# Kernel tuning notes

Hardware: AMD Instinct MI355X
Metric: run time of the kernel (lower is better)

Reference implementation:

```python
import jax, jax.numpy as jnp
import numpy as np

V, H, E, L = 50257, 1024, 1024, 512


def setup_inputs() -> dict:
    key = jax.random.key(0)
    ks = jax.random.split(key, 16)
    s = 0.02  # init scale
    return {
        "input_token": jax.random.randint(ks[0], (1,), 0, V),
        "hidden": jax.random.normal(ks[1], (1, 1, H), jnp.float32),
        "encoder_outputs": jax.random.normal(ks[2], (L, H), jnp.float32),
        "embedding": jax.random.normal(ks[3], (V, E), jnp.float32) * s,
        "attn_w": jax.random.normal(ks[4], (L, H + E), jnp.float32) * s,
        "attn_b": jnp.zeros((L,), jnp.float32),
        "comb_w": jax.random.normal(ks[5], (E, H + E), jnp.float32) * s,
        "comb_b": jnp.zeros((E,), jnp.float32),
        "w_ih": jax.random.normal(ks[6], (3 * H, E), jnp.float32) * s,
        "w_hh": jax.random.normal(ks[7], (3 * H, H), jnp.float32) * s,
        "b_ih": jnp.zeros((3 * H,), jnp.float32),
        "b_hh": jnp.zeros((3 * H,), jnp.float32),
        "out_w": jax.random.normal(ks[8], (V, H), jnp.float32) * s,
        "out_b": jnp.zeros((V,), jnp.float32),
    }


def reference(input_token, hidden, encoder_outputs, embedding, attn_w, attn_b,
              comb_w, comb_b, w_ih, w_hh, b_ih, b_hh, out_w, out_b):
    # embedded = embedding(input).view(1,1,-1); dropout is identity in eval
    emb = embedding[input_token].reshape(1, E)            # [1, E]
    h0 = hidden[0]                                        # [1, H]
    # attention over encoder positions
    attn_logits = jnp.concatenate([emb, h0], axis=1) @ attn_w.T + attn_b  # [1, L]
    attn_weights = jax.nn.softmax(attn_logits, axis=1)
    attn_applied = attn_weights @ encoder_outputs         # [1, H]
    # combine + relu
    x = jnp.concatenate([emb, attn_applied], axis=1) @ comb_w.T + comb_b  # [1, E]
    x = jax.nn.relu(x)
    # single GRU cell step (PyTorch gate order: r, z, n)
    gi = x @ w_ih.T + b_ih                                # [1, 3H]
    gh = h0 @ w_hh.T + b_hh                               # [1, 3H]
    i_r, i_z, i_n = jnp.split(gi, 3, axis=1)
    h_r, h_z, h_n = jnp.split(gh, 3, axis=1)
    r = jax.nn.sigmoid(i_r + h_r)
    z = jax.nn.sigmoid(i_z + h_z)
    n = jnp.tanh(i_n + r * h_n)
    h_new = (1.0 - z) * n + z * h0                        # [1, H]
    # output projection + log softmax
    logits = h_new @ out_w.T + out_b                      # [1, V]
    out = jax.nn.log_softmax(logits, axis=1)
    return out, h_new[None], attn_weights
```

## Files before the change

### kernel.cpp

```cpp
#include <hip/hip_runtime.h>

#define V 50257
#define H 1024
#define E 1024
#define LENC 512
#define GBLK 2048
#define GWAVES (GBLK * 4)

__device__ __forceinline__ float wave_reduce_sum(float v) {
    #pragma unroll
    for (int off = 32; off > 0; off >>= 1)
        v += __shfl_down(v, off, 64);
    return v;
}

__device__ __forceinline__ float dot1024(const float* __restrict__ Wr,
                                         const float4* __restrict__ v4, int lane) {
    const float4* w4 = (const float4*)Wr;
    float acc = 0.f;
    #pragma unroll
    for (int j = 0; j < 4; ++j) {
        float4 w = w4[lane + 64 * j];
        float4 x = v4[lane + 64 * j];
        acc += w.x * x.x + w.y * x.y + w.z * x.z + w.w * x.w;
    }
    return acc;
}

__global__ void stageA_kernel(const float* __restrict__ attn_w,
                              const float* __restrict__ attn_b,
                              const float* __restrict__ w_hh,
                              const float* __restrict__ b_hh,
                              const float* __restrict__ emb_table,
                              const int*   __restrict__ token,
                              const float* __restrict__ hidden,
                              float* __restrict__ alog,
                              float* __restrict__ g,
                              float* __restrict__ aapp) {
    int bx = blockIdx.x;
    int wid = threadIdx.x >> 6, lane = threadIdx.x & 63;
    const float4* h4 = (const float4*)hidden;
    if (bx < 128) {
        int row = bx * 4 + wid;
        const float* Wr = attn_w + (size_t)row * 2048;
        const float4* e4 = (const float4*)(emb_table + (size_t)(*token) * 1024);
        float acc = dot1024(Wr, e4, lane) + dot1024(Wr + 1024, h4, lane);
        acc = wave_reduce_sum(acc);
        if (lane == 0) alog[row] = acc + attn_b[row];
    } else if (bx < 896) {
        int row = (bx - 128) * 4 + wid;
        float acc = dot1024(w_hh + (size_t)row * 1024, h4, lane);
        acc = wave_reduce_sum(acc);
        if (lane == 0) g[3072 + row] = acc + b_hh[row];
    } else {
        int t = threadIdx.x;
        aapp[t] = 0.f; aapp[256 + t] = 0.f; aapp[512 + t] = 0.f; aapp[768 + t] = 0.f;
    }
}

__global__ void stageC_kernel(const float* __restrict__ alog,
                              const float* __restrict__ enc,
                              float* __restrict__ aapp,
                              float* __restrict__ attnw_out) {
    int bx = blockIdx.x;
    int t = threadIdx.x;
    int lane = t & 63, wid = t >> 6;
    __shared__ float eb[512];
    __shared__ float sm[4], ssum[4];
    float a0 = alog[t], a1 = alog[t + 256];
    float m = fmaxf(a0, a1);
    #pragma unroll
    for (int off = 32; off > 0; off >>= 1)
        m = fmaxf(m, __shfl_down(m, off, 64));
    if (lane == 0) sm[wid] = m;
    __syncthreads();
    float M = fmaxf(fmaxf(sm[0], sm[1]), fmaxf(sm[2], sm[3]));
    float e0 = expf(a0 - M), e1 = expf(a1 - M);
    eb[t] = e0; eb[t + 256] = e1;
    float s = wave_reduce_sum(e0 + e1);
    if (lane == 0) ssum[wid] = s;
    __syncthreads();
    float S = ssum[0] + ssum[1] + ssum[2] + ssum[3];
    if (bx == 0) {
        attnw_out[t] = eb[t] / S;
        attnw_out[t + 256] = eb[t + 256] / S;
    }
    int h  = (bx & 3) * 256 + t;
    int l0 = (bx >> 2) * 8;
    float acc = 0.f;
    #pragma unroll
    for (int l = 0; l < 8; ++l)
        acc += eb[l0 + l] * enc[(size_t)(l0 + l) * 1024 + h];
    atomicAdd(&aapp[h], acc / S);
}

__global__ void stageD_kernel(const float* __restrict__ comb_w,
                              const float* __restrict__ comb_b,
                              const float* __restrict__ emb_table,
                              const int*   __restrict__ token,
                              const float* __restrict__ aapp,
                              float* __restrict__ xbuf) {
    int bx = blockIdx.x;
    int wid = threadIdx.x >> 6, lane = threadIdx.x & 63;
    int row = bx * 4 + wid;
    const float* Wr = comb_w + (size_t)row * 2048;
    const float4* e4 = (const float4*)(emb_table + (size_t)(*token) * 1024);
    float acc = dot1024(Wr, e4, lane) + dot1024(Wr + 1024, (const float4*)aapp, lane);
    acc = wave_reduce_sum(acc);
    if (lane == 0) xbuf[row] = fmaxf(acc + comb_b[row], 0.0f);
}

__global__ void stageE_gru_kernel(const float* __restrict__ w_ih,
                                  const float* __restrict__ b_ih,
                                  const float* __restrict__ xbuf,
                                  const float* __restrict__ g,
                                  const float* __restrict__ hidden,
                                  float* __restrict__ hnew_out) {
    int wid = threadIdx.x >> 6, lane = threadIdx.x & 63;
    int j = blockIdx.x * 4 + wid;
    const float4* x4  = (const float4*)xbuf;
    const float4* wr4 = (const float4*)(w_ih + (size_t)j * 1024);
    const float4* wz4 = (const float4*)(w_ih + (size_t)(j + 1024) * 1024);
    const float4* wn4 = (const float4*)(w_ih + (size_t)(j + 2048) * 1024);
    float ar = 0.f, az = 0.f, an = 0.f;
    #pragma unroll
    for (int jj = 0; jj < 4; ++jj) {
        float4 x  = x4[lane + 64 * jj];
        float4 wr = wr4[lane + 64 * jj];
        float4 wz = wz4[lane + 64 * jj];
        float4 wn = wn4[lane + 64 * jj];
        ar += wr.x * x.x + wr.y * x.y + wr.z * x.z + wr.w * x.w;
        az += wz.x * x.x + wz.y * x.y + wz.z * x.z + wz.w * x.w;
        an += wn.x * x.x + wn.y * x.y + wn.z * x.z + wn.w * x.w;
    }
    ar = wave_reduce_sum(ar);
    az = wave_reduce_sum(az);
    an = wave_reduce_sum(an);
    if (lane == 0) {
        float i_r = ar + b_ih[j];
        float i_z = az + b_ih[j + 1024];
        float i_n = an + b_ih[j + 2048];
        float h_r = g[3072 + j], h_z = g[4096 + j], h_n = g[5120 + j];
        float r = 1.0f / (1.0f + expf(-(i_r + h_r)));
        float z = 1.0f / (1.0f + expf(-(i_z + h_z)));
        float n = tanhf(i_n + r * h_n);
        hnew_out[j] = (1.0f - z) * n + z * hidden[j];
    }
}

__global__ void logits_kernel(const float* __restrict__ hnew,
                              const float* __restrict__ out_w,
                              const float* __restrict__ out_b,
                              float* __restrict__ logits,
                              float* __restrict__ part) {
    __shared__ float4 hsm4[256];
    int t = threadIdx.x;
    hsm4[t] = ((const float4*)hnew)[t];
    __syncthreads();
    int wid = t >> 6, lane = t & 63;
    const float4* h4 = (const float4*)hsm4;
    float4 x0 = h4[lane], x1 = h4[lane + 64], x2 = h4[lane + 128], x3 = h4[lane + 192];
    float psum = 0.f;
    for (int row = blockIdx.x * 4 + wid; row < V; row += GWAVES) {
        const float4* w4 = (const float4*)(out_w + (size_t)row * 1024);
        float4 w0 = w4[lane], w1 = w4[lane + 64], w2 = w4[lane + 128], w3 = w4[lane + 192];
        float acc = w0.x * x0.x + w0.y * x0.y + w0.z * x0.z + w0.w * x0.w
                  + w1.x * x1.x + w1.y * x1.y + w1.z * x1.z + w1.w * x1.w
                  + w2.x * x2.x + w2.y * x2.y + w2.z * x2.z + w2.w * x2.w
                  + w3.x * x3.x + w3.y * x3.y + w3.z * x3.z + w3.w * x3.w;
        acc = wave_reduce_sum(acc);
        if (lane == 0) {
            acc += out_b[row];
            logits[row] = acc;
            psum += expf(acc);
        }
    }
    __shared__ float s[4];
    if (lane == 0) s[wid] = psum;
    __syncthreads();
    if (t == 0) part[blockIdx.x] = s[0] + s[1] + s[2] + s[3];
}

__global__ void logsub_kernel(float* __restrict__ out,
                              const float* __restrict__ part) {
    int t = threadIdx.x;
    int lane = t & 63, wid = t >> 6;
    float v = 0.f;
    #pragma unroll
    for (int i = 0; i < 8; ++i) v += part[t + 256 * i];
    v = wave_reduce_sum(v);
    __shared__ float s[4];
    if (lane == 0) s[wid] = v;
    __syncthreads();
    float lse = logf(s[0] + s[1] + s[2] + s[3]);
    int i = blockIdx.x * 256 + t;
    if (i < V) out[i] -= lse;
}

extern "C" void kernel_launch(void* const* d_in, const int* in_sizes, int n_in,
                              void* d_out, int out_size, void* d_ws, size_t ws_size,
                              hipStream_t stream) {
    const int*   token     = (const int*)d_in[0];
    const float* hidden    = (const float*)d_in[1];
    const float* enc       = (const float*)d_in[2];
    const float* emb_table = (const float*)d_in[3];
    const float* attn_w    = (const float*)d_in[4];
    const float* attn_b    = (const float*)d_in[5];
    const float* comb_w    = (const float*)d_in[6];
    const float* comb_b    = (const float*)d_in[7];
    const float* w_ih      = (const float*)d_in[8];
    const float* w_hh      = (const float*)d_in[9];
    const float* b_ih      = (const float*)d_in[10];
    const float* b_hh      = (const float*)d_in[11];
    const float* out_w     = (const float*)d_in[12];
    const float* out_b     = (const float*)d_in[13];

    float* out       = (float*)d_out;
    float* hnew_out  = out + V;
    float* attnw_out = out + V + H;

    float* wsf  = (float*)d_ws;
    float* alog = wsf;
    float* aapp = alog + 512;
    float* xbuf = aapp + 1024;
    float* g    = xbuf + 1024;
    float* part = g + 6144;

    stageA_kernel<<<897, 256, 0, stream>>>(attn_w, attn_b, w_hh, b_hh, emb_table,
                                           token, hidden, alog, g, aapp);
    stageC_kernel<<<256, 256, 0, stream>>>(alog, enc, aapp, attnw_out);
    stageD_kernel<<<256, 256, 0, stream>>>(comb_w, comb_b, emb_table, token, aapp,
                                           xbuf);
    stageE_gru_kernel<<<256, 256, 0, stream>>>(w_ih, b_ih, xbuf, g, hidden,
                                               hnew_out);
    logits_kernel<<<GBLK, 256, 0, stream>>>(hnew_out, out_w, out_b, out, part);
    logsub_kernel<<<(V + 255) / 256, 256, 0, stream>>>(out, part);
}
```

Measured before the change: 56.00 us.

## Fuse decoder stages into one cooperative persistent kernel with atomic flag barriers

Replaces the six separate kernel launches with a single cooperative mega-kernel of 512 blocks. Stages communicate through per-stage atomic counters with hierarchical fan-in and fan-out flags, and blocks spin-wait on these counters. The goal is to remove launch gaps and kernel-boundary drains in a latency-bound decoder step. In exchange it adds a memset, spin-wait barrier overhead, and fewer blocks for the large output projection. The old multi-kernel path is kept as a fallback.

```diff
diff --git a/kernel.cpp b/kernel.cpp
--- a/kernel.cpp
+++ b/kernel.cpp
@@ -4,8 +4,19 @@
 #define H 1024
 #define E 1024
 #define LENC 512
+#define NB 512
+#define NWAVES (NB * 4)
 #define GBLK 2048
-#define GWAVES (GBLK * 4)
+
+#define CSTRIDE 800
+#define F_ALOG 0
+#define F_AAPP 1
+#define F_X    2
+#define F_GI   3
+#define F_H    4
+#define F_LOG  5
+#define NCNT   6
+#define FLAG_INTS (NCNT * CSTRIDE)
 
 __device__ __forceinline__ float wave_reduce_sum(float v) {
     #pragma unroll
@@ -26,6 +37,200 @@
     }
     return acc;
 }
+
+__device__ __forceinline__ void sig(int* flags, int cid, int per_slot) {
+    __syncthreads();
+    if (threadIdx.x == 0) {
+        __threadfence();
+        int* c = flags + cid * CSTRIDE;
+        int old = __hip_atomic_fetch_add(c + (blockIdx.x & 7) * 32, 1,
+                                         __ATOMIC_RELAXED, __HIP_MEMORY_SCOPE_AGENT);
+        if (old == per_slot - 1) {
+            int o2 = __hip_atomic_fetch_add(c + 8 * 32, 1, __ATOMIC_RELAXED,
+                                            __HIP_MEMORY_SCOPE_AGENT);
+            if (o2 == 7) {
+                #pragma unroll
+                for (int r = 0; r < 16; ++r)
+                    __hip_atomic_fetch_add(c + (9 + r) * 32, 1, __ATOMIC_RELAXED,
+                                           __HIP_MEMORY_SCOPE_AGENT);
+            }
+        }
+    }
+}
+
+__device__ __forceinline__ void wtf(int* flags, int cid) {
+    if (threadIdx.x == 0) {
+        int* d = flags + cid * CSTRIDE + (9 + (blockIdx.x & 15)) * 32;
+        while (__hip_atomic_fetch_add(d, 0, __ATOMIC_RELAXED,
+                                      __HIP_MEMORY_SCOPE_AGENT) == 0)
+            __builtin_amdgcn_s_sleep(8);
+    }
+    __syncthreads();
+    __threadfence();
+}
+
+__global__ void __launch_bounds__(256, 2)
+mega_kernel(const int* __restrict__ token, const float* __restrict__ hidden,
+            const float* __restrict__ enc, const float* __restrict__ emb_table,
+            const float* __restrict__ attn_w, const float* __restrict__ attn_b,
+            const float* __restrict__ comb_w, const float* __restrict__ comb_b,
+            const float* __restrict__ w_ih, const float* __restrict__ w_hh,
+            const float* __restrict__ b_ih, const float* __restrict__ b_hh,
+            const float* __restrict__ out_w, const float* __restrict__ out_b,
+            float* __restrict__ out, float* __restrict__ hnew_out,
+            float* __restrict__ attnw_out,
+            float* __restrict__ alog, float* __restrict__ aapp,
+            float* __restrict__ xbuf, float* __restrict__ g,
+            float* __restrict__ part, int* flags) {
+    __shared__ float4 sh4[256];
+    __shared__ float sred[8];
+    float* sh = (float*)sh4;
+
+    const int bx = blockIdx.x, t = threadIdx.x;
+    const int wid = t >> 6, lane = t & 63;
+    const float4* h4 = (const float4*)hidden;
+
+    if (bx < 128) {
+        int row = bx * 4 + wid;
+        const float* Wr = attn_w + (size_t)row * 2048;
+        const float4* e4 = (const float4*)(emb_table + (size_t)(*token) * 1024);
+        float acc = dot1024(Wr, e4, lane) + dot1024(Wr + 1024, h4, lane);
+        acc = wave_reduce_sum(acc);
+        if (lane == 0) alog[row] = acc + attn_b[row];
+        sig(flags, F_ALOG, 16);
+    } else if (bx < 320) {
+        int r0 = ((bx - 128) * 4 + wid) * 4;
+        #pragma unroll
+        for (int i = 0; i < 4; ++i) {
+            int row = r0 + i;
+            float acc = dot1024(w_hh + (size_t)row * 1024, h4, lane);
+            acc = wave_reduce_sum(acc);
+            if (lane == 0) g[3072 + row] = acc + b_hh[row];
+        }
+    }
+
+    if (bx < 32) {
+        wtf(flags, F_ALOG);
+        float a0 = alog[t], a1 = alog[t + 256];
+        float m = fmaxf(a0, a1);
+        #pragma unroll
+        for (int off = 32; off > 0; off >>= 1)
+            m = fmaxf(m, __shfl_down(m, off, 64));
+        if (lane == 0) sred[wid] = m;
+        __syncthreads();
+        float M = fmaxf(fmaxf(sred[0], sred[1]), fmaxf(sred[2], sred[3]));
+        float e0 = expf(a0 - M), e1 = expf(a1 - M);
+        sh[t] = e0; sh[t + 256] = e1;
+        float s = wave_reduce_sum(e0 + e1);
+        if (lane == 0) sred[4 + wid] = s;
+        __syncthreads();
+        float S = sred[4] + sred[5] + sred[6] + sred[7];
+        if (bx == 0) {
+            attnw_out[t] = sh[t] / S;
+            attnw_out[t + 256] = sh[t + 256] / S;
+        }
+        int c  = bx * 32 + (t & 31);
+        int l0 = (t >> 5) * 64;
+        float acc = 0.f;
+        #pragma unroll 8
+        for (int l = 0; l < 64; ++l)
+            acc += sh[l0 + l] * enc[(size_t)(l0 + l) * 1024 + c];
+        sh[512 + t] = acc;
+        __syncthreads();
+        if (t < 32) {
+            float s2 = 0.f;
+            #pragma unroll
+            for (int j = 0; j < 8; ++j) s2 += sh[512 + j * 32 + t];
+            aapp[bx * 32 + t] = s2 / S;
+        }
+        sig(flags, F_AAPP, 4);
+    }
+
+    if (bx < 128) {
+        wtf(flags, F_AAPP);
+        const float4* e4 = (const float4*)(emb_table + (size_t)(*token) * 1024);
+        const float4* a4 = (const float4*)aapp;
+        int r0 = (bx * 4 + wid) * 2;
+        #pragma unroll
+        for (int i = 0; i < 2; ++i) {
+            int row = r0 + i;
+            const float* Wr = comb_w + (size_t)row * 2048;
+            float acc = dot1024(Wr, e4, lane) + dot1024(Wr + 1024, a4, lane);
+            acc = wave_reduce_sum(acc);
+            if (lane == 0) xbuf[row] = fmaxf(acc + comb_b[row], 0.0f);
+        }
+        sig(flags, F_X, 16);
+    }
+
+    if (bx >= 128 && bx < 320) {
+        wtf(flags, F_X);
+        const float4* x4 = (const float4*)xbuf;
+        int r0 = ((bx - 128) * 4 + wid) * 4;
+        #pragma unroll
+        for (int i = 0; i < 4; ++i) {
+            int row = r0 + i;
+            float acc = dot1024(w_ih + (size_t)row * 1024, x4, lane);
+            acc = wave_reduce_sum(acc);
+            if (lane == 0) g[row] = acc + b_ih[row];
+        }
+        sig(flags, F_GI, 24);
+    }
+
+    if (bx >= 320 && bx < 328) {
+        wtf(flags, F_GI);
+        if (t < 128) {
+            int j = (bx - 320) * 128 + t;
+            float i_r = g[j], i_z = g[j + 1024], i_n = g[j + 2048];
+            float h_r = g[3072 + j], h_z = g[4096 + j], h_n = g[5120 + j];
+            float r = 1.0f / (1.0f + expf(-(i_r + h_r)));
+            float z = 1.0f / (1.0f + expf(-(i_z + h_z)));
+            float n = tanhf(i_n + r * h_n);
+            hnew_out[j] = (1.0f - z) * n + z * hidden[j];
+        }
+        sig(flags, F_H, 1);
+    }
+
+    wtf(flags, F_H);
+    sh4[t] = ((const float4*)hnew_out)[t];
+    __syncthreads();
+    {
+        const float4* hh4 = (const float4*)sh4;
+        float4 x0 = hh4[lane], x1 = hh4[lane + 64], x2 = hh4[lane + 128], x3 = hh4[lane + 192];
+        float psum = 0.f;
+        for (int row = bx * 4 + wid; row < V; row += NWAVES) {
+            const float4* w4 = (const float4*)(out_w + (size_t)row * 1024);
+            float4 w0 = w4[lane], w1 = w4[lane + 64], w2 = w4[lane + 128], w3 = w4[lane + 192];
+            float acc = w0.x * x0.x + w0.y * x0.y + w0.z * x0.z + w0.w * x0.w
+                      + w1.x * x1.x + w1.y * x1.y + w1.z * x1.z + w1.w * x1.w
+                      + w2.x * x2.x + w2.y * x2.y + w2.z * x2.z + w2.w * x2.w
+                      + w3.x * x3.x + w3.y * x3.y + w3.z * x3.z + w3.w * x3.w;
+            acc = wave_reduce_sum(acc);
+            if (lane == 0) {
+                acc += out_b[row];
+                out[row] = acc;
+                psum += expf(acc);
+            }
+        }
+        if (lane == 0) sred[wid] = psum;
+        __syncthreads();
+        if (t == 0) part[bx] = sred[0] + sred[1] + sred[2] + sred[3];
+    }
+    sig(flags, F_LOG, 64);
+
+    wtf(flags, F_LOG);
+    {
+        float v = part[t] + part[t + 256];
+        v = wave_reduce_sum(v);
+        if (lane == 0) sred[wid] = v;
+        __syncthreads();
+        if (t == 0) sred[0] = logf(sred[0] + sred[1] + sred[2] + sred[3]);
+        __syncthreads();
+        float lse = sred[0];
+        for (int row = bx * 4 + wid; row < V; row += NWAVES)
+            if (lane == 0) out[row] -= lse;
+    }
+}
+
 
 __global__ void stageA_kernel(const float* __restrict__ attn_w,
                               const float* __restrict__ attn_b,
@@ -161,7 +366,7 @@
     const float4* h4 = (const float4*)hsm4;
     float4 x0 = h4[lane], x1 = h4[lane + 64], x2 = h4[lane + 128], x3 = h4[lane + 192];
     float psum = 0.f;
-    for (int row = blockIdx.x * 4 + wid; row < V; row += GWAVES) {
+    for (int row = blockIdx.x * 4 + wid; row < V; row += GBLK * 4) {
         const float4* w4 = (const float4*)(out_w + (size_t)row * 1024);
         float4 w0 = w4[lane], w1 = w4[lane + 64], w2 = w4[lane + 128], w3 = w4[lane + 192];
         float acc = w0.x * x0.x + w0.y * x0.y + w0.z * x0.z + w0.w * x0.w
@@ -225,6 +430,27 @@
     float* xbuf = aapp + 1024;
     float* g    = xbuf + 1024;
     float* part = g + 6144;
+    int*   flags = (int*)(part + 2048);
+
+    int maxb = 0;
+    hipError_t oerr = hipOccupancyMaxActiveBlocksPerMultiprocessor(
+        &maxb, (const void*)mega_kernel, 256, 0);
+    bool coop = (oerr == hipSuccess) && (maxb * 256 >= NB);
+
+    if (coop) {
+        hipMemsetAsync(flags, 0, FLAG_INTS * sizeof(int), stream);
+        void* args[] = {(void*)&token, (void*)&hidden, (void*)&enc, (void*)&emb_table,
+                        (void*)&attn_w, (void*)&attn_b, (void*)&comb_w, (void*)&comb_b,
+                        (void*)&w_ih, (void*)&w_hh, (void*)&b_ih, (void*)&b_hh,
+                        (void*)&out_w, (void*)&out_b,
+                        (void*)&out, (void*)&hnew_out, (void*)&attnw_out,
+                        (void*)&alog, (void*)&aapp, (void*)&xbuf, (void*)&g,
+                        (void*)&part, (void*)&flags};
+        hipError_t lerr = hipLaunchCooperativeKernel((void*)mega_kernel, dim3(NB),
+                                                     dim3(256), args, 0, stream);
+        if (lerr == hipSuccess) return;
+        (void)hipGetLastError();
+    }
 
     stageA_kernel<<<897, 256, 0, stream>>>(attn_w, attn_b, w_hh, b_hh, emb_table,
                                            token, hidden, alog, g, aapp);
```

Result: slower. 198.7 us (+254.9%).
